# Optimization experiments

Hardware: AMD Instinct MI355X
Metric: run time of the kernel (lower is better)

## Reference

```python
import jax, jax.numpy as jnp
import numpy as np


def setup_inputs() -> dict:
    key = jax.random.key(0)
    k1, k2, k3 = jax.random.split(key, 3)
    N, DIN, DOUT = 8192, 256, 256
    adjacency = jax.random.uniform(k1, (N, N), dtype=jnp.float32)
    input_feature = jax.random.normal(k2, (N, DIN), dtype=jnp.float32)
    weight = jax.random.normal(k3, (DIN, DOUT), dtype=jnp.float32) * (1.0 / np.sqrt(DIN))
    bias = jnp.zeros((DOUT,), dtype=jnp.float32)
    return {"adjacency": adjacency, "input_feature": input_feature,
            "weight": weight, "bias": bias, "l": 1}


def reference(adjacency, input_feature, weight, bias, l):
    # support = X @ W
    support = input_feature @ weight  # [N, DOUT]
    # A = adjacency + l*I ; degrees = rowsum(A) = rowsum(adjacency) + l
    deg = jnp.sum(adjacency, axis=1) + jnp.asarray(l, adjacency.dtype)  # [N]
    # D^{-1/2} with inf (from zero degree) replaced by 0
    d = jnp.where(deg > 0, deg ** -0.5, jnp.zeros_like(deg))  # [N]
    # D @ adjacency @ D  (row scale then col scale of the ORIGINAL adjacency,
    # self-loops only affect the degree, matching the torch code)
    norm_adj = adjacency * d[:, None] * d[None, :]  # [N, N]
    out = norm_adj @ support + bias  # [N, DOUT]
    return out
```

## Files before the change

### kernel.cpp

```cpp
#include <hip/hip_runtime.h>


typedef __attribute__((ext_vector_type(8))) short short8;
typedef __attribute__((ext_vector_type(4))) float f32x4;

#define NN 8192
#define DD 256
#define KCHUNK 2048
#define BK 64
#define NITER (KCHUNK / BK)

__device__ inline unsigned short f2bfu(float x) {
    unsigned int u = __builtin_bit_cast(unsigned int, x);
    u += 0x7fffu + ((u >> 16) & 1u);
    return (unsigned short)(u >> 16);
}
__device__ inline unsigned int f2bf2u(float x, float y) {
    return (unsigned int)f2bfu(x) | ((unsigned int)f2bfu(y) << 16);
}
__device__ inline short8 cvt8(float4 a, float4 b) {
    union { unsigned int i[4]; short8 s; } u;
    u.i[0] = f2bf2u(a.x, a.y);
    u.i[1] = f2bf2u(a.z, a.w);
    u.i[2] = f2bf2u(b.x, b.y);
    u.i[3] = f2bf2u(b.z, b.w);
    return u.s;
}

__device__ inline void gload16(const void* g, void* l) {
    __builtin_amdgcn_global_load_lds(
        (const __attribute__((address_space(1))) unsigned int*)g,
        (__attribute__((address_space(3))) unsigned int*)l, 16, 0, 0);
}

__global__ __launch_bounds__(256) void rowsum_conv(const float* __restrict__ A,
                                                   const int* __restrict__ lp,
                                                   float* __restrict__ d,
                                                   unsigned short* __restrict__ Abf) {
    const int t = threadIdx.x;
    const int rl = t >> 4;
    const int cg = t & 15;
    const int i = blockIdx.x * 16 + rl;
    const int ti = i >> 6;
    const int rt = i & 63;
    const int swz = (rt & 7) << 4;

    const f32x4* Ar = (const f32x4*)(A + (size_t)i * NN);
    char* tb = (char*)Abf + (size_t)ti * 128 * 8192 + rt * 128 + ((8 * cg) ^ swz);

    float s0 = 0.f, s1 = 0.f;
#pragma unroll 4
    for (int k = 0; k < 128; ++k) {
        f32x4 v = __builtin_nontemporal_load(Ar + cg + 16 * k);
        s0 += v[0] + v[1];
        s1 += v[2] + v[3];
        *(uint2*)(tb + (size_t)k * 8192) =
            make_uint2(f2bf2u(v[0], v[1]), f2bf2u(v[2], v[3]));
    }
    float s = s0 + s1;
#pragma unroll
    for (int off = 8; off > 0; off >>= 1) s += __shfl_down(s, off, 16);
    if (cg == 0) {
        float deg = s + (float)(*lp);
        d[i] = deg > 0.f ? rsqrtf(deg) : 0.f;
    }
}

__global__ __launch_bounds__(256) void wtrans_kernel(const float* __restrict__ W,
                                                     unsigned short* __restrict__ WT) {
    __shared__ unsigned short tile[64][65];
    const int tx = threadIdx.x & 63, ty = threadIdx.x >> 6;
    const int i0 = (blockIdx.x & 3) * 64;
    const int n0 = (blockIdx.x >> 2) * 64;
#pragma unroll
    for (int r = ty; r < 64; r += 4)
        tile[r][tx] = f2bfu(W[(size_t)(i0 + r) * DD + n0 + tx]);
    __syncthreads();
#pragma unroll
    for (int r = ty; r < 64; r += 4)
        WT[(size_t)(n0 + r) * DD + i0 + tx] = tile[tx][r];
}

__global__ __launch_bounds__(256) void support_kernel(const float* __restrict__ X,
                                                      const unsigned short* __restrict__ WT,
                                                      const float* __restrict__ d,
                                                      unsigned short* __restrict__ ST) {
    const int j0 = blockIdx.x * 16;
    const int lane = threadIdx.x & 63;
    const int w = threadIdx.x >> 6;
    const int q = lane >> 4;
    const int l15 = lane & 15;
    const int nb = w * 64;

    f32x4 acc[4];
#pragma unroll
    for (int b = 0; b < 4; ++b) acc[b] = (f32x4)(0.f);

    const float* Xbase = X + (size_t)(j0 + l15) * DD + q * 8;
    const unsigned short* Wbase = WT + (size_t)(nb + l15) * DD + q * 8;

#pragma unroll
    for (int k0 = 0; k0 < DD; k0 += 32) {
        const float4* p = (const float4*)(Xbase + k0);
        short8 afr = cvt8(p[0], p[1]);
        short8 bfr[4];
#pragma unroll
        for (int ni = 0; ni < 4; ++ni)
            bfr[ni] = *(const short8*)(Wbase + ni * 16 * DD + k0);
#pragma unroll
        for (int ni = 0; ni < 4; ++ni)
            acc[ni] = __builtin_amdgcn_mfma_f32_16x16x32_bf16(afr, bfr[ni], acc[ni], 0, 0, 0);
    }

    const int j0r = j0 + q * 4;
    float dj[4];
#pragma unroll
    for (int r = 0; r < 4; ++r) dj[r] = d[j0r + r];
#pragma unroll
    for (int ni = 0; ni < 4; ++ni) {
        const int n = nb + ni * 16 + l15;
        unsigned int lo = f2bf2u(acc[ni][0] * dj[0], acc[ni][1] * dj[1]);
        unsigned int hi = f2bf2u(acc[ni][2] * dj[2], acc[ni][3] * dj[3]);
        *(uint2*)(ST + (size_t)n * NN + j0r) = make_uint2(lo, hi);
    }
}

__global__ __launch_bounds__(256) void main_gemm(const unsigned short* __restrict__ Abf,
                                                 const unsigned short* __restrict__ ST,
                                                 float* __restrict__ part) {
    __shared__ __align__(16) unsigned short Abuf[2][4096];

    const int mt = blockIdx.x & 127;
    const int kc = blockIdx.x >> 7;
    const int tid = threadIdx.x;
    const int lane = tid & 63;
    const int w = tid >> 6;
    const int q = lane >> 4;
    const int l15 = lane & 15;
    const int nb = w * 64;
    const int swz = (l15 & 7) << 4;

    const char* Ag = (const char*)Abf + ((size_t)mt * 128 + kc * NITER) * 8192
                     + w * 2048 + lane * 16;
    const unsigned short* Bptr = ST + (size_t)(nb + l15) * NN + kc * KCHUNK + q * 8;

    f32x4 acc[4][4];
#pragma unroll
    for (int a = 0; a < 4; ++a)
#pragma unroll
        for (int b = 0; b < 4; ++b) acc[a][b] = (f32x4)(0.f);

    short8 bfr[2][2][4];

    {
        unsigned short* l0 = &Abuf[0][w * 1024];
        gload16(Ag, l0);
        gload16(Ag + 1024, l0 + 512);
    }
    __builtin_amdgcn_sched_barrier(0);
#pragma unroll
    for (int kk2 = 0; kk2 < 2; ++kk2)
#pragma unroll
        for (int ni = 0; ni < 4; ++ni)
            bfr[0][kk2][ni] = *(const short8*)(Bptr + (size_t)(ni * 16) * NN + kk2 * 32);
    __builtin_amdgcn_sched_barrier(0);

    const char* Ab0 = (const char*)&Abuf[0][0] + l15 * 128;
    const char* Ab1 = (const char*)&Abuf[1][0] + l15 * 128;

#pragma unroll 2
    for (int it = 0; it < NITER; ++it) {
        const int buf = it & 1;
        __asm__ __volatile__("s_waitcnt vmcnt(8)\n\ts_barrier" ::: "memory");

        if (it + 1 < NITER) {
            const char* gn = Ag + (size_t)(it + 1) * 8192;
            unsigned short* ln = &Abuf[buf ^ 1][w * 1024];
            gload16(gn, ln);
            gload16(gn + 1024, ln + 512);
        }
        __builtin_amdgcn_sched_barrier(0);
        if (it + 1 < NITER) {
#pragma unroll
            for (int kk2 = 0; kk2 < 2; ++kk2)
#pragma unroll
                for (int ni = 0; ni < 4; ++ni)
                    bfr[buf ^ 1][kk2][ni] = *(const short8*)(
                        Bptr + (size_t)(ni * 16) * NN + (it + 1) * BK + kk2 * 32);
        }
        __builtin_amdgcn_sched_barrier(0);

        const char* Ab = buf ? Ab1 : Ab0;
#pragma unroll
        for (int kk2 = 0; kk2 < 2; ++kk2) {
            short8 afr[4];
#pragma unroll
            for (int mi = 0; mi < 4; ++mi)
                afr[mi] = *(const short8*)(Ab + mi * 2048 + ((kk2 * 64 + q * 16) ^ swz));
#pragma unroll
            for (int mi = 0; mi < 4; ++mi)
#pragma unroll
                for (int ni = 0; ni < 4; ++ni)
                    acc[mi][ni] = __builtin_amdgcn_mfma_f32_16x16x32_bf16(
                        afr[mi], bfr[buf][kk2][ni], acc[mi][ni], 0, 0, 0);
        }
    }

    float* P = part + (size_t)kc * NN * DD;
#pragma unroll
    for (int mi = 0; mi < 4; ++mi) {
        const int r0 = mt * 64 + mi * 16 + q * 4;
#pragma unroll
        for (int ni = 0; ni < 4; ++ni) {
            const int n = nb + ni * 16 + l15;
#pragma unroll
            for (int rr = 0; rr < 4; ++rr)
                P[(size_t)(r0 + rr) * DD + n] = acc[mi][ni][rr];
        }
    }
}

__global__ __launch_bounds__(256) void reduce_kernel(const float* __restrict__ part,
                                                     const float* __restrict__ d,
                                                     const float* __restrict__ bias,
                                                     float* __restrict__ out) {
    const int idx = blockIdx.x * 256 + threadIdx.x;
    const int i = idx >> 6;
    const int c4 = (idx & 63) << 2;
    const size_t off = (size_t)i * DD + c4;
    const size_t stride = (size_t)NN * DD;
    f32x4 s = *(const f32x4*)(part + off);
    s += *(const f32x4*)(part + stride + off);
    s += *(const f32x4*)(part + 2 * stride + off);
    s += *(const f32x4*)(part + 3 * stride + off);
    const float di = d[i];
    const f32x4 b = *(const f32x4*)(bias + c4);
    s = s * di + b;
    *(f32x4*)(out + off) = s;
}

extern "C" void kernel_launch(void* const* d_in, const int* in_sizes, int n_in,
                              void* d_out, int out_size, void* d_ws, size_t ws_size,
                              hipStream_t stream) {
    const float* A = (const float*)d_in[0];
    const float* X = (const float*)d_in[1];
    const float* W = (const float*)d_in[2];
    const float* bias = (const float*)d_in[3];
    const int* lp = (const int*)d_in[4];
    float* out = (float*)d_out;

    float* d = (float*)d_ws;
    unsigned short* WT = (unsigned short*)((char*)d_ws + 32768);
    unsigned short* ST = (unsigned short*)((char*)d_ws + 32768 + 131072);
    float* part = (float*)((char*)d_ws + 4358144);
    unsigned short* Abf = (unsigned short*)((char*)d_ws + 37912576);
    (void)ws_size;

    rowsum_conv<<<NN / 16, 256, 0, stream>>>(A, lp, d, Abf);
    wtrans_kernel<<<16, 256, 0, stream>>>(W, WT);
    support_kernel<<<NN / 16, 256, 0, stream>>>(X, WT, d, ST);
    main_gemm<<<128 * (NN / KCHUNK), 256, 0, stream>>>(Abf, ST, part);
    reduce_kernel<<<NN * DD / 4 / 256, 256, 0, stream>>>(part, d, bias, out);
}
```

Baseline: 472.1 us.

## Deepen main GEMM prefetch pipeline to two stages with inline-asm B loads

Restructures the main GEMM loop to prefetch A tiles two iterations ahead into a 4-slot LDS ring and to issue B-fragment loads with inline global_load_dwordx4 using immediate offsets after the MFMAs. It also remaps block indices so neighbouring blocks share M tiles across K chunks, and requests two blocks per CU via launch bounds. The aim is to hide global load latency and cut address arithmetic, at the cost of more LDS, more registers and hand-tuned vmcnt waits that must match the exact order in which loads are issued.

```diff
diff --git a/kernel.cpp b/kernel.cpp
--- a/kernel.cpp
+++ b/kernel.cpp
@@ -32,6 +32,10 @@
         (const __attribute__((address_space(1))) unsigned int*)g,
         (__attribute__((address_space(3))) unsigned int*)l, 16, 0, 0);
 }
+
+#define BLOAD(dst, ptr, OFFSTR)                                        \
+    asm volatile("global_load_dwordx4 %0, %1, off offset:" OFFSTR      \
+                 : "=v"(dst) : "v"(ptr))
 
 __global__ __launch_bounds__(256) void rowsum_conv(const float* __restrict__ A,
                                                    const int* __restrict__ lp,
@@ -125,13 +129,14 @@
     }
 }
 
-__global__ __launch_bounds__(256) void main_gemm(const unsigned short* __restrict__ Abf,
-                                                 const unsigned short* __restrict__ ST,
-                                                 float* __restrict__ part) {
-    __shared__ __align__(16) unsigned short Abuf[2][4096];
-
-    const int mt = blockIdx.x & 127;
-    const int kc = blockIdx.x >> 7;
+__global__ __launch_bounds__(256, 2) void main_gemm(const unsigned short* __restrict__ Abf,
+                                                    const unsigned short* __restrict__ ST,
+                                                    float* __restrict__ part) {
+    __shared__ __align__(16) unsigned short Abuf[4][4096];
+
+    const int bid = blockIdx.x;
+    const int kc = (bid & 7) >> 1;
+    const int mt = ((bid >> 3) << 1) | (bid & 1);
     const int tid = threadIdx.x;
     const int lane = tid & 63;
     const int w = tid >> 6;
@@ -142,7 +147,12 @@
 
     const char* Ag = (const char*)Abf + ((size_t)mt * 128 + kc * NITER) * 8192
                      + w * 2048 + lane * 16;
-    const unsigned short* Bptr = ST + (size_t)(nb + l15) * NN + kc * KCHUNK + q * 8;
+
+    const char* Pn[4];
+#pragma unroll
+    for (int ni = 0; ni < 4; ++ni)
+        Pn[ni] = (const char*)ST +
+                 ((size_t)(nb + l15 + ni * 16) * NN + (size_t)kc * KCHUNK + q * 8) * 2;
 
     f32x4 acc[4][4];
 #pragma unroll
@@ -159,38 +169,40 @@
     }
     __builtin_amdgcn_sched_barrier(0);
 #pragma unroll
-    for (int kk2 = 0; kk2 < 2; ++kk2)
-#pragma unroll
-        for (int ni = 0; ni < 4; ++ni)
-            bfr[0][kk2][ni] = *(const short8*)(Bptr + (size_t)(ni * 16) * NN + kk2 * 32);
-    __builtin_amdgcn_sched_barrier(0);
-
-    const char* Ab0 = (const char*)&Abuf[0][0] + l15 * 128;
-    const char* Ab1 = (const char*)&Abuf[1][0] + l15 * 128;
+    for (int ni = 0; ni < 4; ++ni) {
+        BLOAD(bfr[0][0][ni], Pn[ni], "0");
+        BLOAD(bfr[0][1][ni], Pn[ni], "64");
+    }
+    __builtin_amdgcn_sched_barrier(0);
+    {
+        unsigned short* l1 = &Abuf[1][w * 1024];
+        gload16(Ag + 8192, l1);
+        gload16(Ag + 8192 + 1024, l1 + 512);
+    }
+    __builtin_amdgcn_sched_barrier(0);
+#pragma unroll
+    for (int ni = 0; ni < 4; ++ni) {
+        BLOAD(bfr[1][0][ni], Pn[ni], "128");
+        BLOAD(bfr[1][1][ni], Pn[ni], "192");
+    }
+    __builtin_amdgcn_sched_barrier(0);
+
+    const char* AbBase = (const char*)&Abuf[0][0] + l15 * 128;
 
 #pragma unroll 2
-    for (int it = 0; it < NITER; ++it) {
-        const int buf = it & 1;
-        __asm__ __volatile__("s_waitcnt vmcnt(8)\n\ts_barrier" ::: "memory");
-
-        if (it + 1 < NITER) {
-            const char* gn = Ag + (size_t)(it + 1) * 8192;
-            unsigned short* ln = &Abuf[buf ^ 1][w * 1024];
+    for (int it = 0; it < NITER - 2; ++it) {
+        __asm__ __volatile__("s_waitcnt vmcnt(10)\n\ts_barrier" ::: "memory");
+        __builtin_amdgcn_sched_barrier(0);
+
+        {
+            const char* gn = Ag + (size_t)(it + 2) * 8192;
+            unsigned short* ln = &Abuf[(it + 2) & 3][w * 1024];
             gload16(gn, ln);
             gload16(gn + 1024, ln + 512);
         }
         __builtin_amdgcn_sched_barrier(0);
-        if (it + 1 < NITER) {
-#pragma unroll
-            for (int kk2 = 0; kk2 < 2; ++kk2)
-#pragma unroll
-                for (int ni = 0; ni < 4; ++ni)
-                    bfr[buf ^ 1][kk2][ni] = *(const short8*)(
-                        Bptr + (size_t)(ni * 16) * NN + (it + 1) * BK + kk2 * 32);
-        }
-        __builtin_amdgcn_sched_barrier(0);
-
-        const char* Ab = buf ? Ab1 : Ab0;
+
+        const char* Ab = AbBase + ((it & 3) << 13);
 #pragma unroll
         for (int kk2 = 0; kk2 < 2; ++kk2) {
             short8 afr[4];
@@ -202,7 +214,54 @@
 #pragma unroll
                 for (int ni = 0; ni < 4; ++ni)
                     acc[mi][ni] = __builtin_amdgcn_mfma_f32_16x16x32_bf16(
-                        afr[mi], bfr[buf][kk2][ni], acc[mi][ni], 0, 0, 0);
+                        afr[mi], bfr[it & 1][kk2][ni], acc[mi][ni], 0, 0, 0);
+        }
+        __builtin_amdgcn_sched_barrier(0);
+
+#pragma unroll
+        for (int ni = 0; ni < 4; ++ni) {
+            BLOAD(bfr[it & 1][0][ni], Pn[ni], "256");
+            BLOAD(bfr[it & 1][1][ni], Pn[ni], "320");
+        }
+#pragma unroll
+        for (int ni = 0; ni < 4; ++ni) Pn[ni] += 128;
+        __builtin_amdgcn_sched_barrier(0);
+    }
+
+    __asm__ __volatile__("s_waitcnt vmcnt(10)\n\ts_barrier" ::: "memory");
+    __builtin_amdgcn_sched_barrier(0);
+    {
+        const char* Ab = AbBase + (((NITER - 2) & 3) << 13);
+#pragma unroll
+        for (int kk2 = 0; kk2 < 2; ++kk2) {
+            short8 afr[4];
+#pragma unroll
+            for (int mi = 0; mi < 4; ++mi)
+                afr[mi] = *(const short8*)(Ab + mi * 2048 + ((kk2 * 64 + q * 16) ^ swz));
+#pragma unroll
+            for (int mi = 0; mi < 4; ++mi)
+#pragma unroll
+                for (int ni = 0; ni < 4; ++ni)
+                    acc[mi][ni] = __builtin_amdgcn_mfma_f32_16x16x32_bf16(
+                        afr[mi], bfr[0][kk2][ni], acc[mi][ni], 0, 0, 0);
+        }
+    }
+    __asm__ __volatile__("s_waitcnt vmcnt(0)\n\ts_barrier" ::: "memory");
+    __builtin_amdgcn_sched_barrier(0);
+    {
+        const char* Ab = AbBase + (((NITER - 1) & 3) << 13);
+#pragma unroll
+        for (int kk2 = 0; kk2 < 2; ++kk2) {
+            short8 afr[4];
+#pragma unroll
+            for (int mi = 0; mi < 4; ++mi)
+                afr[mi] = *(const short8*)(Ab + mi * 2048 + ((kk2 * 64 + q * 16) ^ swz));
+#pragma unroll
+            for (int mi = 0; mi < 4; ++mi)
+#pragma unroll
+                for (int ni = 0; ni < 4; ++ni)
+                    acc[mi][ni] = __builtin_amdgcn_mfma_f32_16x16x32_bf16(
+                        afr[mi], bfr[1][kk2][ni], acc[mi][ni], 0, 0, 0);
         }
     }
 
```

After: 465.0 us. Within noise of the previous version (-1.5%).
